# Kernel tuning notes

Measured on AMD Instinct MI355X. Metric: run time of the kernel, lower is better.

The kernel has to match this reference:

```python
import jax, jax.numpy as jnp
import numpy as np

B, N, C, K = 8, 4096, 512, 150

def setup_inputs() -> dict:
    key = jax.random.key(0)
    ks = jax.random.split(key, 10)
    std_c = float(np.sqrt(2.0 / C))
    x = jax.random.normal(ks[0], (B, N, C), dtype=jnp.float32)
    Wq = jax.random.normal(ks[1], (K, C), dtype=jnp.float32) * std_c
    bq = jnp.zeros((K,), dtype=jnp.float32)
    Wk = jax.random.normal(ks[2], (K, C), dtype=jnp.float32) * std_c
    bk = jnp.zeros((K,), dtype=jnp.float32)
    Wv = jax.random.normal(ks[3], (C, C), dtype=jnp.float32) * std_c
    bv = jnp.zeros((C,), dtype=jnp.float32)
    # original inits mlp_res to zeros; use small random so output is nontrivial
    Wres = jax.random.normal(ks[4], (C, C), dtype=jnp.float32) * (0.02)
    bres = jnp.zeros((C,), dtype=jnp.float32)
    gamma = jnp.full((1,), 0.5, dtype=jnp.float32)  # original init is 0; nonzero for testing
    return {"x": x, "Wq": Wq, "bq": bq, "Wk": Wk, "bk": bk,
            "Wv": Wv, "bv": bv, "Wres": Wres, "bres": bres, "gamma": gamma}

def reference(x, Wq, bq, Wk, bk, Wv, bv, Wres, bres, gamma):
    # seg_map: (B,N,K); seg_ft: (B,N,K); feats: (B,N,C)
    seg_map = jnp.einsum('bnc,kc->bnk', x, Wq) + bq
    seg_ft = jnp.einsum('bnc,kc->bnk', x, Wk) + bk
    v = jnp.einsum('bnc,dc->bnd', x, Wv) + bv
    # low-rank QK^T -> (B,N,N), unscaled, row softmax
    score = jnp.einsum('bnk,bmk->bnm', seg_map, seg_ft)
    score = jax.nn.softmax(score, axis=-1)
    feats = jnp.einsum('bnm,bmd->bnd', score, v)
    feats = jnp.einsum('bnd,ed->bne', feats, Wres) + bres
    # dropout omitted (inference); gamma-gated residual
    feat_map = gamma * feats + x
    return (seg_map, feat_map)
```

## Files before the change

### kernel.cpp

```cpp
#include <hip/hip_runtime.h>
#include <cstdint>
#include <cstddef>

#define M_ROWS 32768
#define CDIM   512
#define KRANK  150
#define KPAD   160

typedef __bf16 bf16x8 __attribute__((ext_vector_type(8)));
typedef float  f32x4  __attribute__((ext_vector_type(4)));

union U16B { uint4 u; bf16x8 b; };
static __device__ __forceinline__ bf16x8 u2b(uint4 u) { U16B x; x.u = u; return x.b; }

static __device__ __forceinline__ unsigned short f2bf(float f) {
  uint32_t u = __float_as_uint(f);
  u += 0x7fffu + ((u >> 16) & 1u);
  return (unsigned short)(u >> 16);
}

static __device__ __forceinline__ void cvt8(float4 a, float4 b, uint4& h, uint4& l) {
  float v[8] = {a.x, a.y, a.z, a.w, b.x, b.y, b.z, b.w};
  unsigned short hs[8], ls[8];
#pragma unroll
  for (int i = 0; i < 8; ++i) {
    hs[i] = f2bf(v[i]);
    const float hf = __uint_as_float((uint32_t)hs[i] << 16);
    ls[i] = f2bf(v[i] - hf);
  }
  h = *(uint4*)&hs[0];
  l = *(uint4*)&ls[0];
}

static __device__ __forceinline__ void glds16(const void* g, void* l) {
  __builtin_amdgcn_global_load_lds(
      (const __attribute__((address_space(1))) unsigned int*)g,
      (__attribute__((address_space(3))) unsigned int*)l, 16, 0, 0);
}

static __device__ __forceinline__ int sa16f(int row, int k4) {
  return ((row >> 1) << 3) + ((((row & 1) << 2) | k4) ^ ((row >> 1) & 7));
}

__global__ __launch_bounds__(512)
void cvt_w(const float* __restrict__ Wv, const float* __restrict__ Wres,
           const float* __restrict__ Wq, const float* __restrict__ Wk,
           unsigned short* __restrict__ WvC, unsigned short* __restrict__ WresC,
           unsigned short* __restrict__ WqC, unsigned short* __restrict__ WkC)
{
  int job = blockIdx.x;
  const float* W; unsigned short* img; int N;
  if (job < 32)      { W = Wv;   img = WvC;   N = 512; }
  else if (job < 64) { W = Wres; img = WresC; N = 512; job -= 32; }
  else if (job < 80) { W = Wq;   img = WqC;   N = KRANK; job -= 64; }
  else               { W = Wk;   img = WkC;   N = KRANK; job -= 80; }
  const int nt = (N == 512) ? (job >> 4) : 0;
  const int kt = job & 15;

  const int tid = threadIdx.x;
  const int srow = tid >> 2, sk4 = tid & 3;
  const int sa = sa16f(srow, sk4);
  unsigned short* ib = img + (size_t)(nt * 16 + kt) * 16384;
#pragma unroll
  for (int h = 0; h < 2; ++h) {
    const int row = nt * 256 + h * 128 + srow;
    float4 v0 = make_float4(0.f, 0.f, 0.f, 0.f), v1 = v0;
    if (row < N) {
      v0 = *(const float4*)&W[(size_t)row * 512 + kt * 32 + sk4 * 8];
      v1 = *(const float4*)&W[(size_t)row * 512 + kt * 32 + sk4 * 8 + 4];
    }
    uint4 h4, l4; cvt8(v0, v1, h4, l4);
    const int cell = h * 512 + sa;
    *(uint4*)&ib[(size_t)cell * 8]          = h4;
    *(uint4*)&ib[(size_t)(1024 + cell) * 8] = l4;
  }
}

template<int MODE>
__global__ __launch_bounds__(512, 4)
void mgemm_nt(const float* __restrict__ A, const unsigned short* __restrict__ Wimg,
              const float* __restrict__ bias, float* __restrict__ out,
              const float* __restrict__ xres, const float* __restrict__ gammap,
              unsigned short* __restrict__ aux)
{
  __shared__ __align__(16) unsigned short lds[24576];
  const int tid = threadIdx.x;
  const int m0  = blockIdx.y * 128;

  const int srow = tid >> 2, sk4 = tid & 3;
  const int sa16 = sa16f(srow, sk4);
  const float* ap = A + (size_t)(m0 + srow) * 512 + sk4 * 8;

  const int lane = tid & 63, w = tid >> 6;
  const int wm = w >> 2, wn = w & 3;
  const int cq = lane & 15, quad = lane >> 4;
  const int fsub = (((cq & 1) << 2) | quad) ^ (cq >> 1);
  const int a16 = wm * 256 + ((cq >> 1) << 3) + fsub;
  const int b16 = wn * 256 + ((cq >> 1) << 3) + fsub;

  const unsigned short* ibase = Wimg + (size_t)(blockIdx.x * 16) * 16384
                              + (size_t)(w * 64 + lane) * 8;

  f32x4 acc[4][4];
#pragma unroll
  for (int i = 0; i < 4; ++i)
#pragma unroll
    for (int j = 0; j < 4; ++j) acc[i][j] = (f32x4){0.f, 0.f, 0.f, 0.f};

  for (int kt = 0; kt < 512; kt += 32) {
    const float4 av0 = *(const float4*)(ap + kt);
    const float4 av1 = *(const float4*)(ap + kt + 4);
    uint4 ahi, alo;
    cvt8(av0, av1, ahi, alo);

    __syncthreads();
    *(uint4*)&lds[       sa16 * 8] = ahi;
    *(uint4*)&lds[4096 + sa16 * 8] = alo;
    const unsigned short* src = ibase + (size_t)(kt >> 5) * 16384;
#pragma unroll
    for (int c = 0; c < 4; ++c)
      glds16(src + (size_t)c * 4096, &lds[8192 + (c * 512 + w * 64) * 8]);
    __syncthreads();

    bf16x8 ah[4], al_[4];
#pragma unroll
    for (int i = 0; i < 4; ++i) {
      ah[i]  = u2b(*(const uint4*)&lds[       (a16 + i * 64) * 8]);
      al_[i] = u2b(*(const uint4*)&lds[4096 + (a16 + i * 64) * 8]);
    }
#pragma unroll
    for (int j = 0; j < 4; ++j) {
      const bf16x8 bh = u2b(*(const uint4*)&lds[8192  + (b16 + j * 64) * 8]);
      const bf16x8 bl = u2b(*(const uint4*)&lds[16384 + (b16 + j * 64) * 8]);
#pragma unroll
      for (int i = 0; i < 4; ++i) {
        acc[i][j] = __builtin_amdgcn_mfma_f32_16x16x32_bf16(ah[i],  bh, acc[i][j], 0, 0, 0);
        acc[i][j] = __builtin_amdgcn_mfma_f32_16x16x32_bf16(al_[i], bh, acc[i][j], 0, 0, 0);
        acc[i][j] = __builtin_amdgcn_mfma_f32_16x16x32_bf16(ah[i],  bl, acc[i][j], 0, 0, 0);
      }
    }
  }

  const int n0b = blockIdx.x * 256;
  const int mb = m0 + wm * 64 + quad * 4;
  const int nb = n0b + wn * 64 + cq;

  if (MODE == 1) {
    const float g = gammap[0];
#pragma unroll
    for (int j = 0; j < 4; ++j) {
      const float bvj = bias[nb + j * 16];
#pragma unroll
      for (int i = 0; i < 4; ++i) {
#pragma unroll
        for (int r = 0; r < 4; ++r) {
          const size_t off = (size_t)(mb + i * 16 + r) * 512 + (nb + j * 16);
          out[off] = fmaf(g, acc[i][j][r] + bvj, xres[off]);
        }
      }
    }
  } else if (MODE == 4) {
    const int b = m0 >> 12;
    const int key0 = (m0 & 4095) + wm * 64 + quad * 4;
#pragma unroll
    for (int j = 0; j < 4; ++j) {
      const float bvj = bias[nb + j * 16];
      const size_t rowo = (size_t)(b * 512 + nb + j * 16) * 4096;
#pragma unroll
      for (int i = 0; i < 4; ++i) {
        unsigned short o4[4];
#pragma unroll
        for (int r = 0; r < 4; ++r) o4[r] = f2bf(acc[i][j][r] + bvj);
        uint2 o;
        o.x = (unsigned int)o4[0] | ((unsigned int)o4[1] << 16);
        o.y = (unsigned int)o4[2] | ((unsigned int)o4[3] << 16);
        *(uint2*)&aux[rowo + key0 + i * 16] = o;
      }
    }
  } else {
#pragma unroll
    for (int j = 0; j < 4; ++j) {
      const int n = nb + j * 16;
      if (n < KPAD) {
        const float bvj = (n < KRANK) ? bias[n] : 0.f;
#pragma unroll
        for (int i = 0; i < 4; ++i) {
#pragma unroll
          for (int r = 0; r < 4; ++r) {
            const int m = mb + i * 16 + r;
            float v = (n < KRANK) ? (acc[i][j][r] + bvj) : 0.f;
            if (MODE == 2 && n < KRANK) out[(size_t)m * KRANK + n] = v;
            const unsigned short h = f2bf(v);
            aux[(size_t)m * 320 + n] = h;
            const float hf = __uint_as_float(((uint32_t)h) << 16);
            aux[(size_t)m * 320 + 160 + n] = f2bf(v - hf);
          }
        }
      }
    }
  }
}

__global__ __launch_bounds__(512, 2)
void attn_mfma(const unsigned short* __restrict__ Qc,
               const unsigned short* __restrict__ Kc,
               const unsigned short* __restrict__ VT,
               float* __restrict__ O)
{
  __shared__ __align__(16) unsigned short smem[32064];
  unsigned short* klds = smem;
  unsigned short* vtl  = smem + 10496;
  unsigned short* plds = smem + 26944;

  const int bid = blockIdx.x;
  const int b   = bid & 7;
  const int qt  = bid >> 3;
  const int r0  = (b << 12) + qt * 128;

  const int tid  = threadIdx.x;
  const int w    = tid >> 6;
  const int lane = tid & 63;
  const int quad = lane >> 4;
  const int cq   = lane & 15;

  bf16x8 qhi[5], qlo[5];
  {
    const size_t qrow = (size_t)(r0 + w * 16 + cq) * 320;
#pragma unroll
    for (int c = 0; c < 5; ++c) {
      qhi[c] = u2b(*(const uint4*)(Qc + qrow + c * 32 + quad * 8));
      qlo[c] = u2b(*(const uint4*)(Qc + qrow + 160 + c * 32 + quad * 8));
    }
  }

  f32x4 acc4[32];
#pragma unroll
  for (int i = 0; i < 32; ++i) acc4[i] = (f32x4){0.f, 0.f, 0.f, 0.f};
  float mreg[4], lreg[4];
#pragma unroll
  for (int r = 0; r < 4; ++r) { mreg[r] = -3.0e38f; lreg[r] = 0.f; }

  const int vqd = (tid & 3) * 8;
  const int vc  = tid >> 2;
  const int vwb = (tid & 3) * 4112 + vc * 8;
  const int vrb = quad * 4112 + cq * 8;

  const int krow0 = tid / 40,          kc0 = (tid - krow0 * 40) * 8;
  const int krow1 = (tid + 512) / 40,  kc1 = ((tid + 512) - krow1 * 40) * 8;
  const int krow2 = (tid + 1024) / 40, kc2 = ((tid + 1024) - krow2 * 40) * 8;

  uint4 pk0, pk1, pk2, pv0, pv1, pv2, pv3;
  const unsigned short* kbase = Kc + (size_t)(b * 4096) * 320;
  const unsigned short* vbase = VT + ((size_t)(b * 512 + vc)) * 4096 + vqd;
  {
    pk0 = *(const uint4*)(kbase + (size_t)tid * 8);
    pk1 = *(const uint4*)(kbase + (size_t)(tid + 512) * 8);
    if (tid < 256) pk2 = *(const uint4*)(kbase + (size_t)(tid + 1024) * 8);
    pv0 = *(const uint4*)(vbase);
    pv1 = *(const uint4*)(vbase + (size_t)128 * 4096);
    pv2 = *(const uint4*)(vbase + (size_t)256 * 4096);
    pv3 = *(const uint4*)(vbase + (size_t)384 * 4096);
  }

  for (int kt = 0; kt < 128; ++kt) {
    __syncthreads();

    *(uint4*)&klds[krow0 * 328 + kc0] = pk0;
    *(uint4*)&klds[krow1 * 328 + kc1] = pk1;
    if (tid < 256) *(uint4*)&klds[krow2 * 328 + kc2] = pk2;
    *(uint4*)&vtl[vwb]        = pv0;
    *(uint4*)&vtl[vwb + 1024] = pv1;
    *(uint4*)&vtl[vwb + 2048] = pv2;
    *(uint4*)&vtl[vwb + 3072] = pv3;

    __syncthreads();

    {
      const int ktn = (kt < 127) ? kt + 1 : 127;
      pk0 = *(const uint4*)(kbase + (size_t)(ktn * 32 * 320) + (size_t)tid * 8);
      pk1 = *(const uint4*)(kbase + (size_t)(ktn * 32 * 320) + (size_t)(tid + 512) * 8);
      if (tid < 256) pk2 = *(const uint4*)(kbase + (size_t)(ktn * 32 * 320) + (size_t)(tid + 1024) * 8);
      pv0 = *(const uint4*)(vbase + ktn * 32);
      pv1 = *(const uint4*)(vbase + (size_t)128 * 4096 + ktn * 32);
      pv2 = *(const uint4*)(vbase + (size_t)256 * 4096 + ktn * 32);
      pv3 = *(const uint4*)(vbase + (size_t)384 * 4096 + ktn * 32);
    }

    f32x4 S0 = (f32x4){0.f, 0.f, 0.f, 0.f};
    f32x4 S1 = (f32x4){0.f, 0.f, 0.f, 0.f};
    __builtin_amdgcn_s_setprio(1);
#pragma unroll
    for (int c = 0; c < 5; ++c) {
      const int ko = c * 32 + quad * 8;
      const bf16x8 kh0 = u2b(*(const uint4*)&klds[cq * 328 + ko]);
      const bf16x8 kl0 = u2b(*(const uint4*)&klds[cq * 328 + 160 + ko]);
      const bf16x8 kh1 = u2b(*(const uint4*)&klds[(16 + cq) * 328 + ko]);
      const bf16x8 kl1 = u2b(*(const uint4*)&klds[(16 + cq) * 328 + 160 + ko]);
      S0 = __builtin_amdgcn_mfma_f32_16x16x32_bf16(qhi[c], kh0, S0, 0, 0, 0);
      S1 = __builtin_amdgcn_mfma_f32_16x16x32_bf16(qhi[c], kh1, S1, 0, 0, 0);
      S0 = __builtin_amdgcn_mfma_f32_16x16x32_bf16(qhi[c], kl0, S0, 0, 0, 0);
      S1 = __builtin_amdgcn_mfma_f32_16x16x32_bf16(qhi[c], kl1, S1, 0, 0, 0);
      S0 = __builtin_amdgcn_mfma_f32_16x16x32_bf16(qlo[c], kh0, S0, 0, 0, 0);
      S1 = __builtin_amdgcn_mfma_f32_16x16x32_bf16(qlo[c], kh1, S1, 0, 0, 0);
    }
    __builtin_amdgcn_s_setprio(0);

    unsigned short* pw = plds + w * 640;
    float alph[4];
    bool upd = false;
#pragma unroll
    for (int r = 0; r < 4; ++r) {
      const float s0 = S0[r], s1 = S1[r];
      float t = fmaxf(s0, s1);
      t = fmaxf(t, __shfl_xor(t, 1));
      t = fmaxf(t, __shfl_xor(t, 2));
      t = fmaxf(t, __shfl_xor(t, 4));
      t = fmaxf(t, __shfl_xor(t, 8));
      const float mo = mreg[r];
      const bool need = (t > mo + 8.f);
      const float mn = need ? t : mo;
      upd = upd || need;
      const float al = need ? __expf(mo - mn) : 1.f;
      const float p0 = __expf(s0 - mn);
      const float p1 = __expf(s1 - mn);
      float ts = p0 + p1;
      ts += __shfl_xor(ts, 1);
      ts += __shfl_xor(ts, 2);
      ts += __shfl_xor(ts, 4);
      ts += __shfl_xor(ts, 8);
      lreg[r] = lreg[r] * al + ts;
      mreg[r] = mn;
      alph[r] = al;
      const int prow = (quad * 4 + r) * 40;
      pw[prow + cq]      = f2bf(p0);
      pw[prow + 16 + cq] = f2bf(p1);
    }

    if (__any(upd)) {
#pragma unroll
      for (int i = 0; i < 32; ++i) {
        acc4[i][0] *= alph[0]; acc4[i][1] *= alph[1];
        acc4[i][2] *= alph[2]; acc4[i][3] *= alph[3];
      }
    }

    const bf16x8 pa = u2b(*(const uint4*)&pw[cq * 40 + quad * 8]);
    __builtin_amdgcn_s_setprio(1);
#pragma unroll
    for (int i = 0; i < 32; ++i) {
      const bf16x8 vb = u2b(*(const uint4*)&vtl[vrb + i * 128]);
      acc4[i] = __builtin_amdgcn_mfma_f32_16x16x32_bf16(pa, vb, acc4[i], 0, 0, 0);
    }
    __builtin_amdgcn_s_setprio(0);
  }

  float inv[4];
#pragma unroll
  for (int r = 0; r < 4; ++r) inv[r] = 1.f / lreg[r];

  __syncthreads();
  float* ep = (float*)smem + w * 1088;
  const int r0w = r0 + w * 16;
#pragma unroll
  for (int qtr = 0; qtr < 8; ++qtr) {
#pragma unroll
    for (int ii = 0; ii < 4; ++ii)
#pragma unroll
      for (int r = 0; r < 4; ++r)
        ep[(quad * 4 + r) * 68 + ii * 16 + cq] = acc4[qtr * 4 + ii][r] * inv[r];
#pragma unroll
    for (int t = 0; t < 4; ++t) {
      const int flat4 = t * 64 + lane;
      const int row = flat4 >> 4;
      const int c4 = flat4 & 15;
      const float4 val = *(const float4*)&ep[row * 68 + c4 * 4];
      *(float4*)&O[(size_t)(r0w + row) * CDIM + qtr * 64 + c4 * 4] = val;
    }
  }
}

extern "C" void kernel_launch(void* const* d_in, const int* in_sizes, int n_in,
                              void* d_out, int out_size, void* d_ws, size_t ws_size,
                              hipStream_t stream)
{
  const float* x     = (const float*)d_in[0];
  const float* Wq    = (const float*)d_in[1];
  const float* bq    = (const float*)d_in[2];
  const float* Wk    = (const float*)d_in[3];
  const float* bk    = (const float*)d_in[4];
  const float* Wv    = (const float*)d_in[5];
  const float* bv    = (const float*)d_in[6];
  const float* Wres  = (const float*)d_in[7];
  const float* bres  = (const float*)d_in[8];
  const float* gamma = (const float*)d_in[9];

  float* seg_map  = (float*)d_out;
  float* feat_map = seg_map + (size_t)M_ROWS * KRANK;

  unsigned short* Qcomb = (unsigned short*)d_ws;
  unsigned short* Kcomb = Qcomb + (size_t)M_ROWS * 320;
  unsigned short* VTb   = Kcomb + (size_t)M_ROWS * 320;
  float*          feats = (float*)(VTb + (size_t)M_ROWS * CDIM);
  unsigned short* WvC   = (unsigned short*)(feats + (size_t)M_ROWS * CDIM);
  unsigned short* WresC = WvC   + (size_t)2 * 16 * 16384;
  unsigned short* WqC   = WresC + (size_t)2 * 16 * 16384;
  unsigned short* WkC   = WqC   + (size_t)16 * 16384;

  cvt_w<<<dim3(96), dim3(512), 0, stream>>>(Wv, Wres, Wq, Wk, WvC, WresC, WqC, WkC);
  mgemm_nt<2><<<dim3(1, 256), dim3(512), 0, stream>>>(x, WqC, bq, seg_map, nullptr, nullptr, Qcomb);
  mgemm_nt<3><<<dim3(1, 256), dim3(512), 0, stream>>>(x, WkC, bk, nullptr, nullptr, nullptr, Kcomb);
  mgemm_nt<4><<<dim3(2, 256), dim3(512), 0, stream>>>(x, WvC, bv, nullptr, nullptr, nullptr, VTb);
  attn_mfma<<<dim3(256), dim3(512), 0, stream>>>(Qcomb, Kcomb, VTb, feats);
  mgemm_nt<1><<<dim3(2, 256), dim3(512), 0, stream>>>(feats, WresC, bres, feat_map, x, gamma, nullptr);
}
```

Baseline: 771.6 us.

## Split PV work across wave pairs so each V fragment feeds two row tiles

Each wave pair now shares two 16-row P tiles, and each wave covers half of the 512 output columns. Every V fragment loaded from LDS therefore feeds two MFMAs, which halves the V LDS reads per wave. The row-sum reduction is done with an MFMA against a ones vector instead of cross-lane shuffles. Rescale factors, update flags and inverse sums are exchanged through shared memory, which adds an extra __syncthreads per key tile.

```diff
diff --git a/kernel.cpp b/kernel.cpp
--- a/kernel.cpp
+++ b/kernel.cpp
@@ -207,10 +207,13 @@
                const unsigned short* __restrict__ VT,
                float* __restrict__ O)
 {
-  __shared__ __align__(16) unsigned short smem[32064];
+  __shared__ __align__(16) unsigned short smem[32592];
   unsigned short* klds = smem;
   unsigned short* vtl  = smem + 10496;
   unsigned short* plds = smem + 26944;
+  float*    alw   = (float*)(smem + 32064);
+  unsigned* updf  = (unsigned*)(smem + 32320);
+  float*    linvp = (float*)(smem + 32336);
 
   const int bid = blockIdx.x;
   const int b   = bid & 7;
@@ -222,6 +225,8 @@
   const int lane = tid & 63;
   const int quad = lane >> 4;
   const int cq   = lane & 15;
+  const int p    = w >> 1;
+  const int h    = w & 1;
 
   bf16x8 qhi[5], qlo[5];
   {
@@ -243,11 +248,14 @@
   const int vqd = (tid & 3) * 8;
   const int vc  = tid >> 2;
   const int vwb = (tid & 3) * 4112 + vc * 8;
-  const int vrb = quad * 4112 + cq * 8;
+  const int vrb = quad * 4112 + h * 2048 + cq * 8;
 
   const int krow0 = tid / 40,          kc0 = (tid - krow0 * 40) * 8;
   const int krow1 = (tid + 512) / 40,  kc1 = ((tid + 512) - krow1 * 40) * 8;
   const int krow2 = (tid + 1024) / 40, kc2 = ((tid + 1024) - krow2 * 40) * 8;
+
+  uint4 os; os.x = os.y = os.z = os.w = 0x3F803F80u;
+  const bf16x8 vone = u2b(os);
 
   uint4 pk0, pk1, pk2, pv0, pv1, pv2, pv3;
   const unsigned short* kbase = Kc + (size_t)(b * 4096) * 320;
@@ -320,61 +328,94 @@
       const bool need = (t > mo + 8.f);
       const float mn = need ? t : mo;
       upd = upd || need;
-      const float al = need ? __expf(mo - mn) : 1.f;
+      alph[r] = need ? __expf(mo - mn) : 1.f;
+      mreg[r] = mn;
       const float p0 = __expf(s0 - mn);
       const float p1 = __expf(s1 - mn);
-      float ts = p0 + p1;
-      ts += __shfl_xor(ts, 1);
-      ts += __shfl_xor(ts, 2);
-      ts += __shfl_xor(ts, 4);
-      ts += __shfl_xor(ts, 8);
-      lreg[r] = lreg[r] * al + ts;
-      mreg[r] = mn;
-      alph[r] = al;
       const int prow = (quad * 4 + r) * 40;
       pw[prow + cq]      = f2bf(p0);
       pw[prow + 16 + cq] = f2bf(p1);
     }
 
-    if (__any(upd)) {
-#pragma unroll
-      for (int i = 0; i < 32; ++i) {
-        acc4[i][0] *= alph[0]; acc4[i][1] *= alph[1];
-        acc4[i][2] *= alph[2]; acc4[i][3] *= alph[3];
-      }
-    }
-
-    const bf16x8 pa = u2b(*(const uint4*)&pw[cq * 40 + quad * 8]);
+    {
+      const bf16x8 pa_self = u2b(*(const uint4*)&pw[cq * 40 + quad * 8]);
+      f32x4 sum4 = (f32x4){0.f, 0.f, 0.f, 0.f};
+      sum4 = __builtin_amdgcn_mfma_f32_16x16x32_bf16(pa_self, vone, sum4, 0, 0, 0);
+#pragma unroll
+      for (int r = 0; r < 4; ++r) lreg[r] = lreg[r] * alph[r] + sum4[r];
+    }
+    if (cq == 0) {
+#pragma unroll
+      for (int r = 0; r < 4; ++r) alw[w * 16 + quad * 4 + r] = alph[r];
+    }
+    const bool anyu = __any(upd);
+    if (lane == 0) updf[w] = anyu ? 1u : 0u;
+
+    __syncthreads();
+
+    const unsigned short* pb = plds + (2 * p) * 640 + cq * 40 + quad * 8;
+    const bf16x8 pa0 = u2b(*(const uint4*)pb);
+    const bf16x8 pa1 = u2b(*(const uint4*)(pb + 640));
+
+    if (updf[2 * p] | updf[2 * p + 1]) {
+      float aA[4], aB[4];
+#pragma unroll
+      for (int r = 0; r < 4; ++r) {
+        aA[r] = alw[(2 * p) * 16 + quad * 4 + r];
+        aB[r] = alw[(2 * p + 1) * 16 + quad * 4 + r];
+      }
+#pragma unroll
+      for (int ct = 0; ct < 16; ++ct) {
+#pragma unroll
+        for (int r = 0; r < 4; ++r) {
+          acc4[ct][r]      *= aA[r];
+          acc4[16 + ct][r] *= aB[r];
+        }
+      }
+    }
+
     __builtin_amdgcn_s_setprio(1);
 #pragma unroll
-    for (int i = 0; i < 32; ++i) {
-      const bf16x8 vb = u2b(*(const uint4*)&vtl[vrb + i * 128]);
-      acc4[i] = __builtin_amdgcn_mfma_f32_16x16x32_bf16(pa, vb, acc4[i], 0, 0, 0);
+    for (int ct = 0; ct < 16; ++ct) {
+      const bf16x8 vb = u2b(*(const uint4*)&vtl[vrb + ct * 128]);
+      acc4[ct]      = __builtin_amdgcn_mfma_f32_16x16x32_bf16(pa0, vb, acc4[ct], 0, 0, 0);
+      acc4[16 + ct] = __builtin_amdgcn_mfma_f32_16x16x32_bf16(pa1, vb, acc4[16 + ct], 0, 0, 0);
     }
     __builtin_amdgcn_s_setprio(0);
   }
 
-  float inv[4];
-#pragma unroll
-  for (int r = 0; r < 4; ++r) inv[r] = 1.f / lreg[r];
-
+  if (cq == 0) {
+#pragma unroll
+    for (int r = 0; r < 4; ++r) linvp[w * 16 + quad * 4 + r] = 1.f / lreg[r];
+  }
   __syncthreads();
+
+  float invv[2][4];
+#pragma unroll
+  for (int rt = 0; rt < 2; ++rt)
+#pragma unroll
+    for (int r = 0; r < 4; ++r)
+      invv[rt][r] = linvp[(2 * p + rt) * 16 + quad * 4 + r];
+
   float* ep = (float*)smem + w * 1088;
-  const int r0w = r0 + w * 16;
-#pragma unroll
-  for (int qtr = 0; qtr < 8; ++qtr) {
-#pragma unroll
-    for (int ii = 0; ii < 4; ++ii)
-#pragma unroll
-      for (int r = 0; r < 4; ++r)
-        ep[(quad * 4 + r) * 68 + ii * 16 + cq] = acc4[qtr * 4 + ii][r] * inv[r];
-#pragma unroll
-    for (int t = 0; t < 4; ++t) {
-      const int flat4 = t * 64 + lane;
-      const int row = flat4 >> 4;
-      const int c4 = flat4 & 15;
-      const float4 val = *(const float4*)&ep[row * 68 + c4 * 4];
-      *(float4*)&O[(size_t)(r0w + row) * CDIM + qtr * 64 + c4 * 4] = val;
+#pragma unroll
+  for (int rt = 0; rt < 2; ++rt) {
+    const int rowb = r0 + (2 * p + rt) * 16;
+#pragma unroll
+    for (int g = 0; g < 4; ++g) {
+#pragma unroll
+      for (int ii = 0; ii < 4; ++ii)
+#pragma unroll
+        for (int r = 0; r < 4; ++r)
+          ep[(quad * 4 + r) * 68 + ii * 16 + cq] = acc4[rt * 16 + g * 4 + ii][r] * invv[rt][r];
+#pragma unroll
+      for (int t = 0; t < 4; ++t) {
+        const int flat4 = t * 64 + lane;
+        const int row = flat4 >> 4;
+        const int c4 = flat4 & 15;
+        const float4 val = *(const float4*)&ep[row * 68 + c4 * 4];
+        *(float4*)&O[(size_t)(rowb + row) * CDIM + h * 256 + g * 64 + c4 * 4] = val;
+      }
     }
   }
 }
```

New measurement: 769.2 us. No clear change (-0.3%).
